# Optimization experiments

Measured on AMD Instinct MI355X. Metric: run time of the kernel, lower is better.

## Reference

```python
import jax, jax.numpy as jnp
import numpy as np

EPS = 1e-12  # matches torch F.normalize eps


def _gradients(img):
    # forward differences along D, H, W with last slice zeroed (via zero-pad)
    dx = jnp.pad(img[:, :, 1:] - img[:, :, :-1], ((0, 0), (0, 0), (0, 1), (0, 0), (0, 0)))
    dy = jnp.pad(img[:, :, :, 1:] - img[:, :, :, :-1], ((0, 0), (0, 0), (0, 0), (0, 1), (0, 0)))
    dz = jnp.pad(img[:, :, :, :, 1:] - img[:, :, :, :, :-1], ((0, 0), (0, 0), (0, 0), (0, 0), (0, 1)))
    return dx, dy, dz


def _cos(f, t, axis):
    # cosine similarity along `axis` with torch-normalize eps semantics
    fn = f / jnp.maximum(jnp.linalg.norm(f, axis=axis, keepdims=True), EPS)
    tn = t / jnp.maximum(jnp.linalg.norm(t, axis=axis, keepdims=True), EPS)
    return jnp.sum(fn * tn, axis=axis)


def _sploss(f, t, ax_row, ax_col):
    # trace(norm_rows(F) @ norm_rows(T)^T) == sum of row cosine sims; same for cols.
    bc = f.shape[0] * f.shape[1]
    a = jnp.sum(_cos(f, t, ax_col)) / (f.shape[ax_row] * bc)
    b = jnp.sum(_cos(f, t, ax_row)) / (f.shape[ax_col] * bc)
    return -(a + b)


def setup_inputs() -> dict:
    key = jax.random.key(0)
    k1, k2 = jax.random.split(key)
    shape = (2, 1, 160, 160, 160)  # [B, C, D, H, W]
    fake = jax.random.normal(k1, shape, dtype=jnp.float32)
    true = jax.random.normal(k2, shape, dtype=jnp.float32)
    return {"fake": fake, "true": true}


def reference(fake, true):
    fx, fy, fz = _gradients(fake)
    tx, ty, tz = _gradients(true)
    # dim='x' slices are [H, W] -> rows axis 3, cols axis 4
    trace_x = _sploss(fx, tx, 3, 4)
    # dim='y' slices are [D, W] -> rows axis 2, cols axis 4
    trace_y = _sploss(fy, ty, 2, 4)
    # dim='z' slices are [D, H] -> rows axis 2, cols axis 3
    trace_z = _sploss(fz, tz, 2, 3)
    return (trace_x + trace_y + trace_z) / 3.0
```

## Files before the change

### kernel.cpp

```cpp
#include <hip/hip_runtime.h>
#include <math.h>

#define DD 160
#define HH 160
#define WW 160
#define NB 2
#define SLICE (HH * WW)
#define NV 51200
#define Dt 4
#define NDC 40
#define NHC 10
#define HCS 16
#define NTHR 320
#define NBLK (NB * NDC * NHC)
#define NQ (NV / 4)

static constexpr float EPS = 1e-12f;
static constexpr float SCALE = -1.0f / 960.0f;

#define ELEM(v, j) ((j) == 0 ? (v).x : ((j) == 1 ? (v).y : ((j) == 2 ? (v).z : (v).w)))

__global__ void zero_kernel(float* out) {
  if (threadIdx.x == 0) out[0] = 0.0f;
}

__global__ __launch_bounds__(NTHR, 2) void mainS(const float* __restrict__ f,
                                                 const float* __restrict__ t,
                                                 float* __restrict__ P,
                                                 float* __restrict__ out) {
  __shared__ float sw[HCS * 40 * 7];
  __shared__ float sh[8 * 40 * 25];
  __shared__ float red[HCS][6];
  __shared__ float cpad[HCS];
  const int tid = threadIdx.x;
  const int g = tid / 40;
  const int l = tid % 40;
  const int w = 4 * l;
  const int wn = (w + 4 < WW) ? (w + 4) : (WW - 1);
  const int hc = blockIdx.x % NHC;
  const int t2 = blockIdx.x / NHC;
  const int dc = t2 % NDC;
  const int b  = t2 / NDC;
  const int d0 = dc * Dt;
  const int r0 = hc * HCS + g * 2;
  const int r1 = r0 + 1;
  const int r2 = (r1 + 1 < HH) ? (r1 + 1) : (HH - 1);
  const float* fb = f + (size_t)b * DD * SLICE;
  const float* tb = t + (size_t)b * DD * SLICE;
  float* pH = P;
  float* pD = P + (size_t)NHC * 6 * NV;

  float4 S0f = *(const float4*)(fb + (size_t)d0 * SLICE + r0 * WW + w);
  float4 S0t = *(const float4*)(tb + (size_t)d0 * SLICE + r0 * WW + w);
  float4 S1f = *(const float4*)(fb + (size_t)d0 * SLICE + r1 * WW + w);
  float4 S1t = *(const float4*)(tb + (size_t)d0 * SLICE + r1 * WW + w);
  float s0fz = (fb + (size_t)d0 * SLICE + r0 * WW)[wn];
  float s0tz = (tb + (size_t)d0 * SLICE + r0 * WW)[wn];
  float s1fz = (fb + (size_t)d0 * SLICE + r1 * WW)[wn];
  float s1tz = (tb + (size_t)d0 * SLICE + r1 * WW)[wn];

  float aD[48];
#pragma unroll
  for (int c = 0; c < 48; ++c) aD[c] = 0.0f;
  float accCos = 0.0f;

#pragma unroll
  for (int p = 0; p < Dt; ++p) {
    const int d = d0 + p;
    const int dn = (d + 1 < DD) ? (d + 1) : d;
    const float* fS = fb + (size_t)d * SLICE;
    const float* tS = tb + (size_t)d * SLICE;
    const float* fN = fb + (size_t)dn * SLICE;
    const float* tN = tb + (size_t)dn * SLICE;
    const float4 Hf  = *(const float4*)(fS + r2 * WW + w);
    const float4 Ht  = *(const float4*)(tS + r2 * WW + w);
    const float4 D0f = *(const float4*)(fN + r0 * WW + w);
    const float4 D0t = *(const float4*)(tN + r0 * WW + w);
    const float4 D1f = *(const float4*)(fN + r1 * WW + w);
    const float4 D1t = *(const float4*)(tN + r1 * WW + w);
    const float d0fz = (fN + r0 * WW)[wn], d0tz = (tN + r0 * WW)[wn];
    const float d1fz = (fN + r1 * WW)[wn], d1tz = (tN + r1 * WW)[wn];

    float aH[24];
#pragma unroll
    for (int c = 0; c < 24; ++c) aH[c] = 0.0f;

    {
      float xd = 0, xf = 0, xt = 0, yd = 0, yf = 0, yt = 0;
#pragma unroll
      for (int j = 0; j < 4; ++j) {
        const float f0 = ELEM(S0f, j), t0 = ELEM(S0t, j);
        const float gxf = ELEM(D0f, j) - f0, gxt = ELEM(D0t, j) - t0;
        const float gyf = ELEM(S1f, j) - f0, gyt = ELEM(S1t, j) - t0;
        const float fnx = (j < 3) ? ELEM(S0f, j + 1) : s0fz;
        const float tnx = (j < 3) ? ELEM(S0t, j + 1) : s0tz;
        const float gzf = fnx - f0, gzt = tnx - t0;
        xd += gxf * gxt; xf += gxf * gxf; xt += gxt * gxt;
        yd += gyf * gyt; yf += gyf * gyf; yt += gyt * gyt;
        aH[j * 6 + 0] += gxf * gxt; aH[j * 6 + 1] += gxf * gxf; aH[j * 6 + 2] += gxt * gxt;
        aH[j * 6 + 3] += gzf * gzt; aH[j * 6 + 4] += gzf * gzf; aH[j * 6 + 5] += gzt * gzt;
        aD[j * 6 + 0] += gyf * gyt; aD[j * 6 + 1] += gyf * gyf; aD[j * 6 + 2] += gyt * gyt;
        aD[j * 6 + 3] += gzf * gzt; aD[j * 6 + 4] += gzf * gzf; aD[j * 6 + 5] += gzt * gzt;
      }
      float* s = &sw[((g * 2 + 0) * 40 + l) * 7];
      s[0] = xd; s[1] = xf; s[2] = xt; s[3] = yd; s[4] = yf; s[5] = yt;
    }
    {
      float xd = 0, xf = 0, xt = 0, yd = 0, yf = 0, yt = 0;
#pragma unroll
      for (int j = 0; j < 4; ++j) {
        const float f0 = ELEM(S1f, j), t0 = ELEM(S1t, j);
        const float gxf = ELEM(D1f, j) - f0, gxt = ELEM(D1t, j) - t0;
        const float gyf = ELEM(Hf, j) - f0, gyt = ELEM(Ht, j) - t0;
        const float fnx = (j < 3) ? ELEM(S1f, j + 1) : s1fz;
        const float tnx = (j < 3) ? ELEM(S1t, j + 1) : s1tz;
        const float gzf = fnx - f0, gzt = tnx - t0;
        xd += gxf * gxt; xf += gxf * gxf; xt += gxt * gxt;
        yd += gyf * gyt; yf += gyf * gyf; yt += gyt * gyt;
        aH[j * 6 + 0] += gxf * gxt; aH[j * 6 + 1] += gxf * gxf; aH[j * 6 + 2] += gxt * gxt;
        aH[j * 6 + 3] += gzf * gzt; aH[j * 6 + 4] += gzf * gzf; aH[j * 6 + 5] += gzt * gzt;
        aD[(4 + j) * 6 + 0] += gyf * gyt; aD[(4 + j) * 6 + 1] += gyf * gyf; aD[(4 + j) * 6 + 2] += gyt * gyt;
        aD[(4 + j) * 6 + 3] += gzf * gzt; aD[(4 + j) * 6 + 4] += gzf * gzf; aD[(4 + j) * 6 + 5] += gzt * gzt;
      }
      float* s = &sw[((g * 2 + 1) * 40 + l) * 7];
      s[0] = xd; s[1] = xf; s[2] = xt; s[3] = yd; s[4] = yf; s[5] = yt;
    }
    {
      float* s2 = &sh[(g * 40 + l) * 25];
#pragma unroll
      for (int c = 0; c < 24; ++c) s2[c] = aH[c];
    }
    S0f = D0f; S0t = D0t; S1f = D1f; S1t = D1t;
    s0fz = d0fz; s0tz = d0tz; s1fz = d1fz; s1tz = d1tz;

    if (p == Dt - 1) {
#pragma unroll
      for (int r = 0; r < 2; ++r) {
        const int h = r0 + r;
#pragma unroll
        for (int cc = 0; cc < 6; ++cc) {
          float4 o;
          o.x = aD[(r * 4 + 0) * 6 + cc];
          o.y = aD[(r * 4 + 1) * 6 + cc];
          o.z = aD[(r * 4 + 2) * 6 + cc];
          o.w = aD[(r * 4 + 3) * 6 + cc];
          *(float4*)(pD + ((size_t)(dc * 6 + cc)) * NV + b * SLICE + h * 160 + 4 * l) = o;
        }
      }
    }
    __syncthreads();

    if (tid < 240) {
      const int cc = tid / 40, ll = tid % 40;
      float v0 = 0, v1 = 0, v2 = 0, v3 = 0;
#pragma unroll
      for (int gg = 0; gg < 8; ++gg) {
        const float* q = &sh[(gg * 40 + ll) * 25];
        v0 += q[0 * 6 + cc]; v1 += q[1 * 6 + cc]; v2 += q[2 * 6 + cc]; v3 += q[3 * 6 + cc];
      }
      const int bd = b * DD + d;
      float4 o; o.x = v0; o.y = v1; o.z = v2; o.w = v3;
      *(float4*)(pH + ((size_t)(hc * 6 + cc)) * NV + bd * 160 + 4 * ll) = o;
    } else {
      for (int k = tid - 240; k < HCS * 6; k += 80) {
        const int row = k / 6, c = k % 6;
        float s = 0.0f;
#pragma unroll 8
        for (int ll = 0; ll < 40; ++ll) s += sw[(row * 40 + ll) * 7 + c];
        red[row][c] = s;
      }
    }
    __syncthreads();
    if (tid < HCS) {
      const float cx = red[tid][0] / (fmaxf(sqrtf(red[tid][1]), EPS) * fmaxf(sqrtf(red[tid][2]), EPS));
      const float cy = red[tid][3] / (fmaxf(sqrtf(red[tid][4]), EPS) * fmaxf(sqrtf(red[tid][5]), EPS));
      accCos += cx + cy;
    }
  }

  if (tid < HCS) cpad[tid] = accCos;
  __syncthreads();
  if (tid == 0) {
    float s = 0.0f;
#pragma unroll
    for (int i = 0; i < HCS; ++i) s += cpad[i];
    atomicAdd(out, s * SCALE);
  }
}

__global__ __launch_bounds__(256) void finalizeW(const float* __restrict__ P,
                                                 float* __restrict__ out) {
  const float* PH = P;
  const float* PD = P + (size_t)NHC * 6 * NV;
  float c = 0.0f;
  if (blockIdx.x < 100) {
    const int u = blockIdx.x * 256 + threadIdx.x;
    const int type = u / NQ;
    const int vec4 = (u % NQ) * 4;
    float4 dot = {0, 0, 0, 0}, ff = {0, 0, 0, 0}, tt = {0, 0, 0, 0};
    const float* base = PH + (size_t)(type * 3) * NV + vec4;
#pragma unroll
    for (int ch = 0; ch < NHC; ++ch) {
      const float* q = base + (size_t)(ch * 6) * NV;
      const float4 a  = *(const float4*)(q);
      const float4 bb = *(const float4*)(q + (size_t)NV);
      const float4 cv = *(const float4*)(q + 2 * (size_t)NV);
      dot.x += a.x;  dot.y += a.y;  dot.z += a.z;  dot.w += a.w;
      ff.x += bb.x;  ff.y += bb.y;  ff.z += bb.z;  ff.w += bb.w;
      tt.x += cv.x;  tt.y += cv.y;  tt.z += cv.z;  tt.w += cv.w;
    }
    c = dot.x / (fmaxf(sqrtf(ff.x), EPS) * fmaxf(sqrtf(tt.x), EPS))
      + dot.y / (fmaxf(sqrtf(ff.y), EPS) * fmaxf(sqrtf(tt.y), EPS))
      + dot.z / (fmaxf(sqrtf(ff.z), EPS) * fmaxf(sqrtf(tt.z), EPS))
      + dot.w / (fmaxf(sqrtf(ff.w), EPS) * fmaxf(sqrtf(tt.w), EPS));
  } else {
    const int u = (blockIdx.x - 100) * 256 + threadIdx.x;
    const int task = u >> 2, s = u & 3;
    const int type = task / NQ;
    const int vec4 = (task % NQ) * 4;
    float v[12];
#pragma unroll
    for (int i = 0; i < 12; ++i) v[i] = 0.0f;
    const float* base = PD + (size_t)(type * 3) * NV + vec4;
    for (int ch = s * 10; ch < s * 10 + 10; ++ch) {
      const float* q = base + (size_t)(ch * 6) * NV;
      const float4 a  = *(const float4*)(q);
      const float4 bb = *(const float4*)(q + (size_t)NV);
      const float4 cv = *(const float4*)(q + 2 * (size_t)NV);
      v[0] += a.x;  v[1] += a.y;  v[2]  += a.z;  v[3]  += a.w;
      v[4] += bb.x; v[5] += bb.y; v[6]  += bb.z; v[7]  += bb.w;
      v[8] += cv.x; v[9] += cv.y; v[10] += cv.z; v[11] += cv.w;
    }
#pragma unroll
    for (int i = 0; i < 12; ++i) {
      v[i] += __shfl_xor(v[i], 1);
      v[i] += __shfl_xor(v[i], 2);
    }
    if (s == 0) {
      c = v[0] / (fmaxf(sqrtf(v[4]), EPS) * fmaxf(sqrtf(v[8]),  EPS))
        + v[1] / (fmaxf(sqrtf(v[5]), EPS) * fmaxf(sqrtf(v[9]),  EPS))
        + v[2] / (fmaxf(sqrtf(v[6]), EPS) * fmaxf(sqrtf(v[10]), EPS))
        + v[3] / (fmaxf(sqrtf(v[7]), EPS) * fmaxf(sqrtf(v[11]), EPS));
    }
  }
#pragma unroll
  for (int m = 32; m >= 1; m >>= 1) c += __shfl_xor(c, m);
  __shared__ float part[4];
  if ((threadIdx.x & 63) == 0) part[threadIdx.x >> 6] = c;
  __syncthreads();
  if (threadIdx.x == 0) atomicAdd(out, (part[0] + part[1] + part[2] + part[3]) * SCALE);
}

extern "C" void kernel_launch(void* const* d_in, const int* in_sizes, int n_in,
                              void* d_out, int out_size, void* d_ws, size_t ws_size,
                              hipStream_t stream) {
  const float* fk = (const float*)d_in[0];
  const float* tr = (const float*)d_in[1];
  float* outp = (float*)d_out;
  float* P = (float*)d_ws;

  hipLaunchKernelGGL(zero_kernel, dim3(1), dim3(64), 0, stream, outp);
  hipLaunchKernelGGL(mainS, dim3(NBLK), dim3(NTHR), 0, stream, fk, tr, P, outp);
  hipLaunchKernelGGL(finalizeW, dim3(500), dim3(256), 0, stream, P, outp);
}
```

Baseline: 140.9 us.

## Store per-row partial sums in fp16 shared memory and raise occupancy target

Per-row H-direction partial products are now packed as half2 into shared memory instead of fp32, which roughly halves that buffer and drops the separate 24-float accumulator array. The two row loops are merged so per-column partials are summed in registers before being stored. Launch bounds go from 2 to 5 blocks per SIMD to raise occupancy. Converting partial sums to fp16 loses precision and can overflow on large gradients, which risks exceeding the accuracy tolerance, and the tighter register budget may cause spills.

Result: slower. 271.8 us (+93.0%).

```diff
diff --git a/kernel.cpp b/kernel.cpp
--- a/kernel.cpp
+++ b/kernel.cpp
@@ -1,4 +1,5 @@
 #include <hip/hip_runtime.h>
+#include <hip/hip_fp16.h>
 #include <math.h>
 
 #define DD 160
@@ -24,12 +25,17 @@
   if (threadIdx.x == 0) out[0] = 0.0f;
 }
 
-__global__ __launch_bounds__(NTHR, 2) void mainS(const float* __restrict__ f,
+static __device__ __forceinline__ unsigned pack_h2(float lo, float hi) {
+  __half2 h = __halves2half2(__float2half_rn(lo), __float2half_rn(hi));
+  return *(unsigned*)&h;
+}
+
+__global__ __launch_bounds__(NTHR, 5) void mainS(const float* __restrict__ f,
                                                  const float* __restrict__ t,
                                                  float* __restrict__ P,
                                                  float* __restrict__ out) {
   __shared__ float sw[HCS * 40 * 7];
-  __shared__ float sh[8 * 40 * 25];
+  __shared__ unsigned shu[NTHR * 13];
   __shared__ float red[HCS][6];
   __shared__ float cpad[HCS];
   const int tid = threadIdx.x;
@@ -81,58 +87,53 @@
     const float d0fz = (fN + r0 * WW)[wn], d0tz = (tN + r0 * WW)[wn];
     const float d1fz = (fN + r1 * WW)[wn], d1tz = (tN + r1 * WW)[wn];
 
-    float aH[24];
-#pragma unroll
-    for (int c = 0; c < 24; ++c) aH[c] = 0.0f;
-
-    {
-      float xd = 0, xf = 0, xt = 0, yd = 0, yf = 0, yt = 0;
-#pragma unroll
-      for (int j = 0; j < 4; ++j) {
+    float xd0 = 0, xf0 = 0, xt0 = 0, yd0 = 0, yf0 = 0, yt0 = 0;
+    float xd1 = 0, xf1 = 0, xt1 = 0, yd1 = 0, yf1 = 0, yt1 = 0;
+
+#pragma unroll
+    for (int j = 0; j < 4; ++j) {
+      float a0, a1, a2, a3, a4, a5;
+      {
         const float f0 = ELEM(S0f, j), t0 = ELEM(S0t, j);
         const float gxf = ELEM(D0f, j) - f0, gxt = ELEM(D0t, j) - t0;
         const float gyf = ELEM(S1f, j) - f0, gyt = ELEM(S1t, j) - t0;
         const float fnx = (j < 3) ? ELEM(S0f, j + 1) : s0fz;
         const float tnx = (j < 3) ? ELEM(S0t, j + 1) : s0tz;
         const float gzf = fnx - f0, gzt = tnx - t0;
-        xd += gxf * gxt; xf += gxf * gxf; xt += gxt * gxt;
-        yd += gyf * gyt; yf += gyf * gyf; yt += gyt * gyt;
-        aH[j * 6 + 0] += gxf * gxt; aH[j * 6 + 1] += gxf * gxf; aH[j * 6 + 2] += gxt * gxt;
-        aH[j * 6 + 3] += gzf * gzt; aH[j * 6 + 4] += gzf * gzf; aH[j * 6 + 5] += gzt * gzt;
+        xd0 += gxf * gxt; xf0 += gxf * gxf; xt0 += gxt * gxt;
+        yd0 += gyf * gyt; yf0 += gyf * gyf; yt0 += gyt * gyt;
+        a0 = gxf * gxt; a1 = gxf * gxf; a2 = gxt * gxt;
+        a3 = gzf * gzt; a4 = gzf * gzf; a5 = gzt * gzt;
         aD[j * 6 + 0] += gyf * gyt; aD[j * 6 + 1] += gyf * gyf; aD[j * 6 + 2] += gyt * gyt;
         aD[j * 6 + 3] += gzf * gzt; aD[j * 6 + 4] += gzf * gzf; aD[j * 6 + 5] += gzt * gzt;
       }
-      float* s = &sw[((g * 2 + 0) * 40 + l) * 7];
-      s[0] = xd; s[1] = xf; s[2] = xt; s[3] = yd; s[4] = yf; s[5] = yt;
-    }
-    {
-      float xd = 0, xf = 0, xt = 0, yd = 0, yf = 0, yt = 0;
-#pragma unroll
-      for (int j = 0; j < 4; ++j) {
+      {
         const float f0 = ELEM(S1f, j), t0 = ELEM(S1t, j);
         const float gxf = ELEM(D1f, j) - f0, gxt = ELEM(D1t, j) - t0;
         const float gyf = ELEM(Hf, j) - f0, gyt = ELEM(Ht, j) - t0;
         const float fnx = (j < 3) ? ELEM(S1f, j + 1) : s1fz;
         const float tnx = (j < 3) ? ELEM(S1t, j + 1) : s1tz;
         const float gzf = fnx - f0, gzt = tnx - t0;
-        xd += gxf * gxt; xf += gxf * gxf; xt += gxt * gxt;
-        yd += gyf * gyt; yf += gyf * gyf; yt += gyt * gyt;
-        aH[j * 6 + 0] += gxf * gxt; aH[j * 6 + 1] += gxf * gxf; aH[j * 6 + 2] += gxt * gxt;
-        aH[j * 6 + 3] += gzf * gzt; aH[j * 6 + 4] += gzf * gzf; aH[j * 6 + 5] += gzt * gzt;
+        xd1 += gxf * gxt; xf1 += gxf * gxf; xt1 += gxt * gxt;
+        yd1 += gyf * gyt; yf1 += gyf * gyf; yt1 += gyt * gyt;
+        a0 += gxf * gxt; a1 += gxf * gxf; a2 += gxt * gxt;
+        a3 += gzf * gzt; a4 += gzf * gzf; a5 += gzt * gzt;
         aD[(4 + j) * 6 + 0] += gyf * gyt; aD[(4 + j) * 6 + 1] += gyf * gyf; aD[(4 + j) * 6 + 2] += gyt * gyt;
         aD[(4 + j) * 6 + 3] += gzf * gzt; aD[(4 + j) * 6 + 4] += gzf * gzf; aD[(4 + j) * 6 + 5] += gzt * gzt;
       }
-      float* s = &sw[((g * 2 + 1) * 40 + l) * 7];
-      s[0] = xd; s[1] = xf; s[2] = xt; s[3] = yd; s[4] = yf; s[5] = yt;
+      unsigned* su = &shu[tid * 13 + j * 3];
+      su[0] = pack_h2(a0, a1);
+      su[1] = pack_h2(a2, a3);
+      su[2] = pack_h2(a4, a5);
     }
     {
-      float* s2 = &sh[(g * 40 + l) * 25];
-#pragma unroll
-      for (int c = 0; c < 24; ++c) s2[c] = aH[c];
+      float* s = &sw[((g * 2 + 0) * 40 + l) * 7];
+      s[0] = xd0; s[1] = xf0; s[2] = xt0; s[3] = yd0; s[4] = yf0; s[5] = yt0;
+      float* s1 = &sw[((g * 2 + 1) * 40 + l) * 7];
+      s1[0] = xd1; s1[1] = xf1; s1[2] = xt1; s1[3] = yd1; s1[4] = yf1; s1[5] = yt1;
     }
     S0f = D0f; S0t = D0t; S1f = D1f; S1t = D1t;
     s0fz = d0fz; s0tz = d0tz; s1fz = d1fz; s1tz = d1tz;
-
     if (p == Dt - 1) {
 #pragma unroll
       for (int r = 0; r < 2; ++r) {
@@ -152,11 +153,15 @@
 
     if (tid < 240) {
       const int cc = tid / 40, ll = tid % 40;
+      const __half* hp = (const __half*)shu;
       float v0 = 0, v1 = 0, v2 = 0, v3 = 0;
 #pragma unroll
       for (int gg = 0; gg < 8; ++gg) {
-        const float* q = &sh[(gg * 40 + ll) * 25];
-        v0 += q[0 * 6 + cc]; v1 += q[1 * 6 + cc]; v2 += q[2 * 6 + cc]; v3 += q[3 * 6 + cc];
+        const __half* q = hp + (gg * 40 + ll) * 26;
+        v0 += __half2float(q[0 * 6 + cc]);
+        v1 += __half2float(q[1 * 6 + cc]);
+        v2 += __half2float(q[2 * 6 + cc]);
+        v3 += __half2float(q[3 * 6 + cc]);
       }
       const int bd = b * DD + d;
       float4 o; o.x = v0; o.y = v1; o.z = v2; o.w = v3;
```
